# Optimization experiments

Measured on AMD Instinct MI355X. Metric: run time of the kernel, lower is better.

The kernel has to match this reference:

```python
import jax, jax.numpy as jnp
import numpy as np

B, T, C = 2, 2048, 1024
H = 16
HD = C // H

def setup_inputs() -> dict:
    key = jax.random.key(0)
    ks = jax.random.split(key, 5)
    scale = 0.02
    return {
        "x": jax.random.normal(ks[0], (B, T, C), jnp.float32),
        "w_attn": jax.random.normal(ks[1], (3 * C, C), jnp.float32) * scale,
        "b_attn": jnp.zeros((3 * C,), jnp.float32),
        "w_proj": jax.random.normal(ks[2], (C, C), jnp.float32) * scale,
        "b_proj": jnp.zeros((C,), jnp.float32),
    }

def reference(x, w_attn, b_attn, w_proj, b_proj):
    Bx, Tx, Cx = x.shape
    # qkv projection (torch Linear: x @ W^T + b)
    qkv = x @ w_attn.T + b_attn                     # [B,T,3C]
    q, k, v = jnp.split(qkv, 3, axis=2)
    # [B,T,C] -> [B,H,T,hd]
    def to_heads(t):
        return t.reshape(Bx, Tx, H, HD).transpose(0, 2, 1, 3)
    q, k, v = to_heads(q), to_heads(k), to_heads(v)
    scores = jnp.einsum('bhqd,bhkd->bhqk', q, k) / np.sqrt(HD).astype(jnp.float32)
    causal_mask = jnp.triu(jnp.ones((Tx, Tx), bool), k=1)   # True above diagonal
    scores = jnp.where(causal_mask, -jnp.inf, scores)
    attn = jax.nn.softmax(scores, axis=-1)
    y = jnp.einsum('bhqk,bhkd->bhqd', attn, v)      # [B,H,T,hd]
    y = y.transpose(0, 2, 1, 3).reshape(Bx, Tx, Cx)
    return y @ w_proj.T + b_proj
```

## Files before the change

### kernel.cpp

```cpp
#include <hip/hip_runtime.h>
#include <hip/hip_bf16.h>

using bf16 = __hip_bfloat16;

typedef __bf16 bf16x8 __attribute__((ext_vector_type(8)));
typedef __bf16 bf16x4v __attribute__((ext_vector_type(4)));
typedef float  float4v __attribute__((ext_vector_type(4)));

#define MFMA16x16x32(a, b, c) __builtin_amdgcn_mfma_f32_16x16x32_bf16((a), (b), (c), 0, 0, 0)

#if __has_builtin(__builtin_amdgcn_exp2f)
#define EXP2F(x) __builtin_amdgcn_exp2f(x)
#else
#define EXP2F(x) exp2f(x)
#endif

#define T_SEQ 2048
#define NHEAD 16
#define CDIM  1024
#define HD3   3072

__device__ __forceinline__ void async_copy16(const void* g, void* l) {
    __builtin_amdgcn_global_load_lds(
        (__attribute__((address_space(1))) unsigned int*)g,
        (__attribute__((address_space(3))) unsigned int*)l,
        16, 0, 0);
}

__global__ __launch_bounds__(256) void detect_dtype_kernel(
    const unsigned short* __restrict__ xs, int* __restrict__ flag)
{
    __shared__ int red[256];
    int cnt = 0;
    for (int i = threadIdx.x; i < 16384; i += 256) {
        const unsigned short u = xs[i];
        const int e = (u >> 7) & 0xFF;
        if (e == 0xFF || (e != 0 && e < 0x60)) cnt++;
    }
    red[threadIdx.x] = cnt;
    __syncthreads();
    for (int s = 128; s > 0; s >>= 1) {
        if (threadIdx.x < s) red[threadIdx.x] += red[threadIdx.x + s];
        __syncthreads();
    }
    if (threadIdx.x == 0) flag[0] = (red[0] > 100) ? 1 : 0;
}

__global__ __launch_bounds__(256) void convert_f32_kernel(
    const float* __restrict__ x, const float* __restrict__ wa,
    const float* __restrict__ wp,
    bf16* __restrict__ xb, bf16* __restrict__ wab, bf16* __restrict__ wpb,
    const int* __restrict__ flag)
{
    if (flag[0] == 0) return;
    const int stride = gridDim.x * 256;
    for (int i = blockIdx.x * 256 + threadIdx.x; i < 8388608; i += stride) {
        if (i < 4194304)      xb[i] = __float2bfloat16(x[i]);
        else if (i < 7340032) wab[i - 4194304] = __float2bfloat16(wa[i - 4194304]);
        else                  wpb[i - 7340032] = __float2bfloat16(wp[i - 7340032]);
    }
}

template<int JF>
__global__ __launch_bounds__(256) void gemm_nt_lds_t(
    const void* __restrict__ Araw, const bf16* __restrict__ Aconv,
    const void* __restrict__ Braw, const bf16* __restrict__ Bconv,
    const void* __restrict__ biasraw, void* __restrict__ Cv,
    int M, int N, int K, const int* __restrict__ flag, int is_final,
    int scale_q, int swz)
{
    const bool f32 = (flag[0] != 0);
    const bf16* A = f32 ? Aconv : (const bf16*)Araw;
    const bf16* B = f32 ? Bconv : (const bf16*)Braw;

    __shared__ bf16 As[128 * 64];
    __shared__ bf16 Bs[JF * 32 * 64];

    const int tid  = threadIdx.x;
    const int lane = tid & 63;
    const int wave = tid >> 6;
    const int wm = wave & 1, wn = wave >> 1;
    const int c = lane & 15, g = lane >> 4;

    int bx = blockIdx.x, by = blockIdx.y;
    if (swz) {
        const int nwg = gridDim.x * gridDim.y;
        const int lin = by * gridDim.x + bx;
        const int nl  = (lin & 7) * (nwg >> 3) + (lin >> 3);
        bx = nl % gridDim.x;
        by = nl / gridDim.x;
    }
    const int bm = bx * 128;
    const int bn = by * (JF * 32);

    const int srow = tid >> 3;
    const int slc  = ((tid & 7) ^ (srow & 7)) * 8;
    const bf16* gA = A + (size_t)(bm + srow) * K + slc;
    const bf16* gB = B + (size_t)(bn + srow) * K + slc;

    float4v acc[4][JF] = {};

    for (int k0 = 0; k0 < K; k0 += 64) {
        __syncthreads();
#pragma unroll
        for (int q = 0; q < 4; ++q)
            async_copy16(gA + k0 + (size_t)(q * 32) * K, As + q * 2048 + tid * 8);
#pragma unroll
        for (int q = 0; q < JF; ++q)
            async_copy16(gB + k0 + (size_t)(q * 32) * K, Bs + q * 2048 + tid * 8);
        __syncthreads();

#pragma unroll
        for (int kk = 0; kk < 2; ++kk) {
            bf16x8 af[4], bfr[JF];
#pragma unroll
            for (int i = 0; i < 4; ++i)
                af[i]  = *(const bf16x8*)&As[(wm * 64 + i * 16 + c) * 64 +
                                             (((kk * 4 + g) ^ (c & 7)) * 8)];
#pragma unroll
            for (int j = 0; j < JF; ++j)
                bfr[j] = *(const bf16x8*)&Bs[(wn * (JF * 16) + j * 16 + c) * 64 +
                                             (((kk * 4 + g) ^ (c & 7)) * 8)];
#pragma unroll
            for (int i = 0; i < 4; ++i)
#pragma unroll
                for (int j = 0; j < JF; ++j)
                    acc[i][j] = MFMA16x16x32(af[i], bfr[j], acc[i][j]);
        }
    }

    const bool f32o = is_final && f32;
    bf16*  Cb = (bf16*)Cv;
    float* Cf = (float*)Cv;

#pragma unroll
    for (int i = 0; i < 4; ++i) {
        const int row = bm + wm * 64 + i * 16 + g * 4;
#pragma unroll
        for (int j = 0; j < JF; ++j) {
            const int col = bn + wn * (JF * 16) + j * 16 + c;
            const float bv = f32 ? ((const float*)biasraw)[col]
                                 : __bfloat162float(((const bf16*)biasraw)[col]);
            const float sc = (scale_q && col < 1024) ? 0.18033688f : 1.0f;
            if (f32o) {
#pragma unroll
                for (int t = 0; t < 4; ++t)
                    Cf[(size_t)(row + t) * N + col] = (acc[i][j][t] + bv) * sc;
            } else {
#pragma unroll
                for (int t = 0; t < 4; ++t)
                    Cb[(size_t)(row + t) * N + col] =
                        __float2bfloat16((acc[i][j][t] + bv) * sc);
            }
        }
    }
}

__global__ __launch_bounds__(256) void attn_mfma(
    const bf16* __restrict__ qkv, bf16* __restrict__ y)
{
    __shared__ __bf16 Ks[2][128 * 64];
    __shared__ __bf16 Vt[2][64 * 128];

    const int tid  = threadIdx.x;
    const int lane = tid & 63;
    const int w    = tid >> 6;
    const int c    = lane & 15;
    const int g    = lane >> 4;

    const int i    = blockIdx.x;
    const int role = i >> 8;
    const int bhl  = i & 7;
    const int t5   = (i & 255) >> 3;
    const int j    = t5 >> 2;
    const int bh   = ((t5 & 3) << 3) | bhl;
    const int qblk = role ? j : (15 - j);
    const int bb   = bh >> 4;
    const int h    = bh & 15;
    const size_t base = (size_t)bb * T_SEQ * HD3 + (size_t)h * 64;

    const int krow = tid >> 3;
    const int klc  = ((tid & 7) ^ (krow & 7)) * 8;
    const int kq   = tid & 31;
    const int dgv  = tid >> 5;
    const int vchunk = (kq >> 3) * 4 + (kq & 3);
    const int vlow   = ((kq >> 2) & 1) * 4;

    const bf16* kgbase = qkv + base + 1024;
    const bf16* vgbase = qkv + base + 2048;

    bf16x8 ones;
#pragma unroll
    for (int ii = 0; ii < 8; ++ii) ones[ii] = (__bf16)1.0f;

    const int q0 = qblk * 128;
    const int qw = q0 + w * 32;

    bf16x8 qf[2][2];
#pragma unroll
    for (int a = 0; a < 2; ++a)
#pragma unroll
        for (int kf2 = 0; kf2 < 2; ++kf2)
            qf[a][kf2] = *(const bf16x8*)(qkv + base
                + (size_t)(qw + a * 16 + c) * HD3 + kf2 * 32 + g * 8);

    float4v o[2][4] = {};
    float4v ol[2] = {};

#pragma unroll
    for (int q = 0; q < 4; ++q)
        async_copy16(kgbase + (size_t)(q * 32 + krow) * HD3 + klc,
                     &Ks[0][q * 2048 + tid * 8]);
    {
        bf16x8 vr[4];
#pragma unroll
        for (int r = 0; r < 4; ++r)
            vr[r] = *(const bf16x8*)(vgbase + (size_t)(kq * 4 + r) * HD3 + dgv * 8);
#pragma unroll
        for (int jj = 0; jj < 8; ++jj) {
            const int d = dgv * 8 + jj;
            bf16x4v pk;
#pragma unroll
            for (int r = 0; r < 4; ++r) pk[r] = vr[r][jj];
            *(bf16x4v*)&Vt[0][d * 128 + ((vchunk ^ (d & 7)) << 3) + vlow] = pk;
        }
    }
    __syncthreads();

    int b = 0;
    for (int kt = 0; kt <= q0; kt += 128, b ^= 1) {
        const bool more = (kt + 128 <= q0);
        bf16x8 vr[4];
        if (more) {
#pragma unroll
            for (int q = 0; q < 4; ++q)
                async_copy16(kgbase + (size_t)(kt + 128 + q * 32 + krow) * HD3 + klc,
                             &Ks[b ^ 1][q * 2048 + tid * 8]);
#pragma unroll
            for (int r = 0; r < 4; ++r)
                vr[r] = *(const bf16x8*)(vgbase + (size_t)(kt + 128 + kq * 4 + r) * HD3 + dgv * 8);
        }

#pragma unroll
        for (int hf = 0; hf < 2; ++hf) {
            if (kt + hf * 64 > qw + 31) continue;

            float4v sacc[2][4] = {};
            __builtin_amdgcn_s_setprio(1);
#pragma unroll
            for (int jb = 0; jb < 4; ++jb) {
                const int key = hf * 64 + jb * 16 + c;
                bf16x8 a0 = *(const bf16x8*)&Ks[b][key * 64 + ((g ^ (c & 7)) * 8)];
                bf16x8 a1 = *(const bf16x8*)&Ks[b][key * 64 + (((4 + g) ^ (c & 7)) * 8)];
#pragma unroll
                for (int a = 0; a < 2; ++a) {
                    sacc[a][jb] = MFMA16x16x32(a0, qf[a][0], sacc[a][jb]);
                    sacc[a][jb] = MFMA16x16x32(a1, qf[a][1], sacc[a][jb]);
                }
            }
            __builtin_amdgcn_s_setprio(0);
            bf16x8 pf[2][2];
#pragma unroll
            for (int a = 0; a < 2; ++a) {
                const int qmin = qw + a * 16;
                if (kt + hf * 64 + 63 > qmin) {
                    const int query = qmin + c;
#pragma unroll
                    for (int jb = 0; jb < 4; ++jb) {
                        const int kb = kt + hf * 64 + jb * 16 + g * 4;
#pragma unroll
                        for (int t = 0; t < 4; ++t)
                            if (kb + t > query) sacc[a][jb][t] = -1e30f;
                    }
                }
#pragma unroll
                for (int jb = 0; jb < 4; ++jb)
#pragma unroll
                    for (int t = 0; t < 4; ++t)
                        sacc[a][jb][t] = EXP2F(sacc[a][jb][t]);
#pragma unroll
                for (int lkf = 0; lkf < 2; ++lkf) {
                    bf16x8 pk;
#pragma unroll
                    for (int jj = 0; jj < 8; ++jj)
                        pk[jj] = (__bf16)sacc[a][lkf * 2 + (jj >> 2)][jj & 3];
                    pf[a][lkf] = pk;
                }
            }
            __builtin_amdgcn_s_setprio(1);
#pragma unroll
            for (int lkf = 0; lkf < 2; ++lkf) {
                const int kf = hf * 2 + lkf;
                ol[0] = MFMA16x16x32(ones, pf[0][lkf], ol[0]);
                ol[1] = MFMA16x16x32(ones, pf[1][lkf], ol[1]);
#pragma unroll
                for (int dn = 0; dn < 4; ++dn) {
                    const int d = dn * 16 + c;
                    bf16x8 vf = *(const bf16x8*)
                        &Vt[b][d * 128 + (((kf * 4 + g) ^ (d & 7)) << 3)];
                    o[0][dn] = MFMA16x16x32(vf, pf[0][lkf], o[0][dn]);
                    o[1][dn] = MFMA16x16x32(vf, pf[1][lkf], o[1][dn]);
                }
            }
            __builtin_amdgcn_s_setprio(0);
        }

        if (more) {
#pragma unroll
            for (int jj = 0; jj < 8; ++jj) {
                const int d = dgv * 8 + jj;
                bf16x4v pk;
#pragma unroll
                for (int r = 0; r < 4; ++r) pk[r] = vr[r][jj];
                *(bf16x4v*)&Vt[b ^ 1][d * 128 + ((vchunk ^ (d & 7)) << 3) + vlow] = pk;
            }
        }
        __syncthreads();
    }

#pragma unroll
    for (int a = 0; a < 2; ++a) {
        const float linv = 1.f / ol[a].x;
        const int q = qw + a * 16 + c;
        const size_t yb = ((size_t)bb * T_SEQ + q) * CDIM + h * 64;
#pragma unroll
        for (int dn = 0; dn < 4; ++dn) {
            bf16x4v ov;
#pragma unroll
            for (int t = 0; t < 4; ++t)
                ov[t] = (__bf16)(o[a][dn][t] * linv);
            *(bf16x4v*)&y[yb + dn * 16 + g * 4] = ov;
        }
    }
}

extern "C" void kernel_launch(void* const* d_in, const int* in_sizes, int n_in,
                              void* d_out, int out_size, void* d_ws, size_t ws_size,
                              hipStream_t stream)
{
    const int M = 4096;
    char* ws = (char*)d_ws;

    int*  flag = (int*)ws;
    bf16* xb   = (bf16*)(ws + 256);
    bf16* wab  = (bf16*)(ws + 8388864);
    bf16* wpb  = (bf16*)(ws + 14680320);
    bf16* qkv  = (bf16*)(ws + 16777472);
    bf16* yb   = (bf16*)(ws + 41943296);

    detect_dtype_kernel<<<1, 256, 0, stream>>>((const unsigned short*)d_in[0], flag);

    convert_f32_kernel<<<512, 256, 0, stream>>>(
        (const float*)d_in[0], (const float*)d_in[1], (const float*)d_in[3],
        xb, wab, wpb, flag);

    {
        dim3 grid(M / 128, 3072 / 128);
        gemm_nt_lds_t<4><<<grid, 256, 0, stream>>>(d_in[0], xb, d_in[1], wab,
                                                   d_in[2], qkv, M, 3072, 1024,
                                                   flag, 0, 1, 1);
    }
    {
        attn_mfma<<<512, 256, 0, stream>>>(qkv, yb);
    }
    {
        dim3 grid(M / 128, 1024 / 64);
        gemm_nt_lds_t<2><<<grid, 256, 0, stream>>>(yb, yb, d_in[3], wpb,
                                                   d_in[4], d_out, M, 1024, 1024,
                                                   flag, 1, 0, 1);
    }
    (void)in_sizes; (void)n_in; (void)out_size; (void)ws_size;
}
```

Before: 212.2 us.

## Use 8 waves per attention block with 16 queries each and split K/V staging

Doubles the attention block to 512 threads so each wave handles 16 query rows instead of 32, halving per-wave accumulators and MFMA work per key tile. The first 256 threads stage K via async LDS copies while the other 256 load and transpose V, instead of every thread doing both. This aims to raise wave-level parallelism and latency hiding and to lower register pressure. In exchange, each K/V fragment read from LDS now feeds fewer MFMAs, and more waves must meet at each barrier.

```diff
diff --git a/kernel.cpp b/kernel.cpp
--- a/kernel.cpp
+++ b/kernel.cpp
@@ -156,7 +156,7 @@
     }
 }
 
-__global__ __launch_bounds__(256) void attn_mfma(
+__global__ __launch_bounds__(512) void attn_mfma(
     const bf16* __restrict__ qkv, bf16* __restrict__ y)
 {
     __shared__ __bf16 Ks[2][128 * 64];
@@ -179,10 +179,12 @@
     const int h    = bh & 15;
     const size_t base = (size_t)bb * T_SEQ * HD3 + (size_t)h * 64;
 
-    const int krow = tid >> 3;
-    const int klc  = ((tid & 7) ^ (krow & 7)) * 8;
-    const int kq   = tid & 31;
-    const int dgv  = tid >> 5;
+    const bool kstage = (tid < 256);
+    const int st   = tid & 255;
+    const int krow = st >> 3;
+    const int klc  = ((st & 7) ^ (krow & 7)) * 8;
+    const int kq   = st & 31;
+    const int dgv  = st >> 5;
     const int vchunk = (kq >> 3) * 4 + (kq & 3);
     const int vlow   = ((kq >> 2) & 1) * 4;
 
@@ -194,24 +196,23 @@
     for (int ii = 0; ii < 8; ++ii) ones[ii] = (__bf16)1.0f;
 
     const int q0 = qblk * 128;
-    const int qw = q0 + w * 32;
-
-    bf16x8 qf[2][2];
-#pragma unroll
-    for (int a = 0; a < 2; ++a)
-#pragma unroll
-        for (int kf2 = 0; kf2 < 2; ++kf2)
-            qf[a][kf2] = *(const bf16x8*)(qkv + base
-                + (size_t)(qw + a * 16 + c) * HD3 + kf2 * 32 + g * 8);
-
-    float4v o[2][4] = {};
-    float4v ol[2] = {};
-
-#pragma unroll
-    for (int q = 0; q < 4; ++q)
-        async_copy16(kgbase + (size_t)(q * 32 + krow) * HD3 + klc,
-                     &Ks[0][q * 2048 + tid * 8]);
-    {
+    const int qw = q0 + w * 16;
+
+    bf16x8 qf[2];
+#pragma unroll
+    for (int kf2 = 0; kf2 < 2; ++kf2)
+        qf[kf2] = *(const bf16x8*)(qkv + base
+            + (size_t)(qw + c) * HD3 + kf2 * 32 + g * 8);
+
+    float4v o[4] = {};
+    float4v ol = {};
+
+    if (kstage) {
+#pragma unroll
+        for (int q = 0; q < 4; ++q)
+            async_copy16(kgbase + (size_t)(q * 32 + krow) * HD3 + klc,
+                         &Ks[0][q * 2048 + st * 8]);
+    } else {
         bf16x8 vr[4];
 #pragma unroll
         for (int r = 0; r < 4; ++r)
@@ -232,80 +233,78 @@
         const bool more = (kt + 128 <= q0);
         bf16x8 vr[4];
         if (more) {
-#pragma unroll
-            for (int q = 0; q < 4; ++q)
-                async_copy16(kgbase + (size_t)(kt + 128 + q * 32 + krow) * HD3 + klc,
-                             &Ks[b ^ 1][q * 2048 + tid * 8]);
-#pragma unroll
-            for (int r = 0; r < 4; ++r)
-                vr[r] = *(const bf16x8*)(vgbase + (size_t)(kt + 128 + kq * 4 + r) * HD3 + dgv * 8);
+            if (kstage) {
+#pragma unroll
+                for (int q = 0; q < 4; ++q)
+                    async_copy16(kgbase + (size_t)(kt + 128 + q * 32 + krow) * HD3 + klc,
+                                 &Ks[b ^ 1][q * 2048 + st * 8]);
+            } else {
+#pragma unroll
+                for (int r = 0; r < 4; ++r)
+                    vr[r] = *(const bf16x8*)(vgbase + (size_t)(kt + 128 + kq * 4 + r) * HD3 + dgv * 8);
+            }
         }
 
 #pragma unroll
         for (int hf = 0; hf < 2; ++hf) {
-            if (kt + hf * 64 > qw + 31) continue;
-
-            float4v sacc[2][4] = {};
+            if (kt + hf * 64 > qw + 15) continue;
+
+            float4v sacc[4] = {};
             __builtin_amdgcn_s_setprio(1);
 #pragma unroll
             for (int jb = 0; jb < 4; ++jb) {
                 const int key = hf * 64 + jb * 16 + c;
                 bf16x8 a0 = *(const bf16x8*)&Ks[b][key * 64 + ((g ^ (c & 7)) * 8)];
                 bf16x8 a1 = *(const bf16x8*)&Ks[b][key * 64 + (((4 + g) ^ (c & 7)) * 8)];
-#pragma unroll
-                for (int a = 0; a < 2; ++a) {
-                    sacc[a][jb] = MFMA16x16x32(a0, qf[a][0], sacc[a][jb]);
-                    sacc[a][jb] = MFMA16x16x32(a1, qf[a][1], sacc[a][jb]);
-                }
+                sacc[jb] = MFMA16x16x32(a0, qf[0], sacc[jb]);
+                sacc[jb] = MFMA16x16x32(a1, qf[1], sacc[jb]);
             }
             __builtin_amdgcn_s_setprio(0);
-            bf16x8 pf[2][2];
-#pragma unroll
-            for (int a = 0; a < 2; ++a) {
-                const int qmin = qw + a * 16;
-                if (kt + hf * 64 + 63 > qmin) {
-                    const int query = qmin + c;
+
+            bf16x8 pf[2];
+            {
+                if (kt + hf * 64 + 63 > qw) {
+                    const int query = qw + c;
 #pragma unroll
                     for (int jb = 0; jb < 4; ++jb) {
                         const int kb = kt + hf * 64 + jb * 16 + g * 4;
 #pragma unroll
                         for (int t = 0; t < 4; ++t)
-                            if (kb + t > query) sacc[a][jb][t] = -1e30f;
+                            if (kb + t > query) sacc[jb][t] = -1e30f;
                     }
                 }
 #pragma unroll
                 for (int jb = 0; jb < 4; ++jb)
 #pragma unroll
                     for (int t = 0; t < 4; ++t)
-                        sacc[a][jb][t] = EXP2F(sacc[a][jb][t]);
+                        sacc[jb][t] = EXP2F(sacc[jb][t]);
 #pragma unroll
                 for (int lkf = 0; lkf < 2; ++lkf) {
                     bf16x8 pk;
 #pragma unroll
                     for (int jj = 0; jj < 8; ++jj)
-                        pk[jj] = (__bf16)sacc[a][lkf * 2 + (jj >> 2)][jj & 3];
-                    pf[a][lkf] = pk;
+                        pk[jj] = (__bf16)sacc[lkf * 2 + (jj >> 2)][jj & 3];
+                    pf[lkf] = pk;
                 }
             }
+
             __builtin_amdgcn_s_setprio(1);
 #pragma unroll
             for (int lkf = 0; lkf < 2; ++lkf) {
                 const int kf = hf * 2 + lkf;
-                ol[0] = MFMA16x16x32(ones, pf[0][lkf], ol[0]);
-                ol[1] = MFMA16x16x32(ones, pf[1][lkf], ol[1]);
+                ol = MFMA16x16x32(ones, pf[lkf], ol);
 #pragma unroll
                 for (int dn = 0; dn < 4; ++dn) {
                     const int d = dn * 16 + c;
                     bf16x8 vf = *(const bf16x8*)
                         &Vt[b][d * 128 + (((kf * 4 + g) ^ (d & 7)) << 3)];
-                    o[0][dn] = MFMA16x16x32(vf, pf[0][lkf], o[0][dn]);
-                    o[1][dn] = MFMA16x16x32(vf, pf[1][lkf], o[1][dn]);
+                    o[dn] = MFMA16x16x32(vf, pf[lkf], o[dn]);
                 }
             }
             __builtin_amdgcn_s_setprio(0);
         }
 
-        if (more) {
+        if (more && !kstage) {
 #pragma unroll
             for (int jj = 0; jj < 8; ++jj) {
                 const int d = dgv * 8 + jj;
@@ -318,17 +317,16 @@
         __syncthreads();
     }
 
-#pragma unroll
-    for (int a = 0; a < 2; ++a) {
-        const float linv = 1.f / ol[a].x;
-        const int q = qw + a * 16 + c;
+    {
+        const float linv = 1.f / ol.x;
+        const int q = qw + c;
         const size_t yb = ((size_t)bb * T_SEQ + q) * CDIM + h * 64;
 #pragma unroll
         for (int dn = 0; dn < 4; ++dn) {
             bf16x4v ov;
 #pragma unroll
             for (int t = 0; t < 4; ++t)
-                ov[t] = (__bf16)(o[a][dn][t] * linv);
+                ov[t] = (__bf16)(o[dn][t] * linv);
             *(bf16x4v*)&y[yb + dn * 16 + g * 4] = ov;
         }
     }
@@ -361,7 +359,7 @@
                                                    flag, 0, 1, 1);
     }
     {
-        attn_mfma<<<512, 256, 0, stream>>>(qkv, yb);
+        attn_mfma<<<512, 512, 0, stream>>>(qkv, yb);
     }
     {
         dim3 grid(M / 128, 1024 / 64);
```

Result: faster. 199.4 us (-6.1%).
